# Kernel tuning notes

Measured on AMD Instinct MI355X. Metric: run time of the kernel, lower is better.

The kernel has to match this reference:

```python
import jax, jax.numpy as jnp
import numpy as np
from jax import lax

B, N, T, F_IN = 16, 500, 256, 8
H, K, OUT = 64, 3, 1
EPS = 1e-5


def setup_inputs() -> dict:
    key = jax.random.key(0)
    ks = jax.random.split(key, 20)
    def xavier(k, shape):
        fan_in, fan_out = shape[-2], shape[-1]
        lim = np.sqrt(6.0 / (fan_in + fan_out))
        return jax.random.uniform(k, shape, jnp.float32, -lim, lim)
    inp = {
        'x': jax.random.normal(ks[0], (B, N, T, F_IN), jnp.float32),
        'adj': jax.random.uniform(ks[1], (N, N), jnp.float32),
        # temporal conv layer 1: in=F_IN, layer 2: in=H; kernel (1,K), OIHW
        'conv_w1': jax.random.normal(ks[2], (H, F_IN, 1, K), jnp.float32) * 0.1,
        'conv_b1': jnp.zeros((H,), jnp.float32),
        'conv_w2': jax.random.normal(ks[3], (H, H, 1, K), jnp.float32) * 0.05,
        'conv_b2': jnp.zeros((H,), jnp.float32),
        # graph conv weights (in,out) + bias
        'gcn_w1': xavier(ks[4], (H, H)),
        'gcn_b1': jnp.zeros((H,), jnp.float32),
        'gcn_w2': xavier(ks[5], (H, H)),
        'gcn_b2': jnp.zeros((H,), jnp.float32),
        # batchnorm (eval mode: running stats)
        'bn_g1': jnp.ones((H,), jnp.float32),
        'bn_be1': jnp.zeros((H,), jnp.float32),
        'bn_m1': jax.random.normal(ks[6], (H,), jnp.float32) * 0.1,
        'bn_v1': jnp.ones((H,), jnp.float32),
        'bn_g2': jnp.ones((H,), jnp.float32),
        'bn_be2': jnp.zeros((H,), jnp.float32),
        'bn_m2': jax.random.normal(ks[7], (H,), jnp.float32) * 0.1,
        'bn_v2': jnp.ones((H,), jnp.float32),
        # output MLP H -> H//2 -> OUT
        'out_w1': xavier(ks[8], (H, H // 2)),
        'out_bb1': jnp.zeros((H // 2,), jnp.float32),
        'out_w2': xavier(ks[9], (H // 2, OUT)),
        'out_bb2': jnp.zeros((OUT,), jnp.float32),
    }
    return inp


def _layer(x, adj, cw, cb, gw, gb, bg, bb, bm, bv):
    # x: (B, C_in, N, T)
    x = lax.conv_general_dilated(
        x, cw, window_strides=(1, 1), padding=[(0, 0), (K // 2, K // 2)],
        dimension_numbers=('NCHW', 'OIHW', 'NCHW'))
    x = jax.nn.relu(x + cb[None, :, None, None])           # (B,H,N,T)
    # batched graph conv over all timesteps at once
    s = jnp.einsum('bcnt,ch->bhnt', x, gw)                 # support = x @ W
    x = jnp.einsum('mn,bhnt->bhmt', adj, s) + gb[None, :, None, None]
    x = jax.nn.relu(x)
    # batchnorm2d eval over channel dim
    x = (x - bm[None, :, None, None]) * (bg / jnp.sqrt(bv + EPS))[None, :, None, None] + bb[None, :, None, None]
    return x  # dropout is identity in eval


def reference(x, adj, conv_w1, conv_b1, conv_w2, conv_b2,
              gcn_w1, gcn_b1, gcn_w2, gcn_b2,
              bn_g1, bn_be1, bn_m1, bn_v1,
              bn_g2, bn_be2, bn_m2, bn_v2,
              out_w1, out_bb1, out_w2, out_bb2):
    h = jnp.transpose(x, (0, 3, 1, 2))                      # (B,F_in,N,T)
    h = _layer(h, adj, conv_w1, conv_b1, gcn_w1, gcn_b1, bn_g1, bn_be1, bn_m1, bn_v1)
    h = _layer(h, adj, conv_w2, conv_b2, gcn_w2, gcn_b2, bn_g2, bn_be2, bn_m2, bn_v2)
    h = h.mean(axis=-1)                                     # (B,H,N)
    h = jnp.transpose(h, (0, 2, 1))                         # (B,N,H)
    h = jax.nn.relu(h @ out_w1 + out_bb1)
    return h @ out_w2 + out_bb2                             # (B,N,OUT)
```

## Files before the change

kernel.cpp:

```cpp
#include <hip/hip_runtime.h>
#include <hip/hip_bf16.h>


#define BB 16
#define NN 500
#define TT 256
#define FIN 8
#define HH 64

using bf16 = __hip_bfloat16;
typedef __attribute__((ext_vector_type(8))) short short8;
typedef __attribute__((ext_vector_type(4))) short short4v;
typedef __attribute__((ext_vector_type(4))) float f32x4;

static __device__ __forceinline__ short bf16bits(float v) {
    __hip_bfloat16 h = __float2bfloat16(v);
    return *reinterpret_cast<short*>(&h);
}

__global__ __launch_bounds__(256) void k_prep_adj(
    const float* __restrict__ adj, bf16* __restrict__ adjb)
{
    int i = blockIdx.x * 256 + threadIdx.x;
    if (i < 512 * 512) {
        int r = i >> 9, c = i & 511;
        float v = (r < NN && c < NN) ? adj[r * NN + c] : 0.f;
        adjb[i] = __float2bfloat16(v);
    }
}

__global__ __launch_bounds__(256) void k_prep_weights(
    const float* __restrict__ cw1, const float* __restrict__ gw1,
    const float* __restrict__ w2,  const float* __restrict__ gw2,
    bf16* __restrict__ wA1, bf16* __restrict__ gA1,
    bf16* __restrict__ wA2, bf16* __restrict__ gA2)
{
    int i = blockIdx.x * 256 + threadIdx.x;
    if (i < 2048) {
        int h = i >> 5, kp = i & 31, kk = kp >> 3, f = kp & 7;
        wA1[i] = __float2bfloat16(kk < 3 ? cw1[(h * 8 + f) * 3 + kk] : 0.f);
    } else if (i < 6144) {
        int j = i - 2048, h = j >> 6, c = j & 63;
        gA1[j] = __float2bfloat16(gw1[c * 64 + h]);
    } else if (i < 18432) {
        int j = i - 6144, kk = j / 4096, r = j & 4095, co = r >> 6, ci = r & 63;
        wA2[j] = __float2bfloat16(w2[(co * 64 + ci) * 3 + kk]);
    } else if (i < 22528) {
        int j = i - 18432, h = j >> 6, c = j & 63;
        gA2[j] = __float2bfloat16(gw2[c * 64 + h]);
    }
}

__global__ __launch_bounds__(256) void k_conv_mfma1(
    const float* __restrict__ x, const bf16* __restrict__ wA1,
    const bf16* __restrict__ gA1, const float* __restrict__ cb,
    bf16* __restrict__ s_out)
{
    __shared__ __align__(16) short xs[256 * 64];

    const int tid = threadIdx.x;
    const int n = blockIdx.x, lb = blockIdx.y;
    const int lane = tid & 63, w = tid >> 6;
    const int lr = lane & 15, kg = lane >> 4;
    const int t0w = w * 64;

    {
        const float4* gx = (const float4*)(x + (size_t)(lb * NN + n) * (TT * FIN) + tid * 8);
        float4 a = gx[0], b = gx[1];
        short8 v;
        v[0] = bf16bits(a.x); v[1] = bf16bits(a.y); v[2] = bf16bits(a.z); v[3] = bf16bits(a.w);
        v[4] = bf16bits(b.x); v[5] = bf16bits(b.y); v[6] = bf16bits(b.z); v[7] = bf16bits(b.w);
        const int t = tid;
        *(short8*)((char*)xs + t * 128 + (16 ^ ((t & 7) << 4))) = v;
        if (t < 255)
            *(short8*)((char*)xs + (t + 1) * 128 + (0 ^ (((t + 1) & 7) << 4))) = v;
        if (t > 0)
            *(short8*)((char*)xs + (t - 1) * 128 + (32 ^ (((t - 1) & 7) << 4))) = v;
        short8 z = {0, 0, 0, 0, 0, 0, 0, 0};
        *(short8*)((char*)xs + t * 128 + (48 ^ ((t & 7) << 4))) = z;
        if (t == 0)   *(short8*)((char*)xs + 0 * 128 + (0 ^ 0)) = z;
        if (t == 255) *(short8*)((char*)xs + 255 * 128 + (32 ^ ((255 & 7) << 4))) = z;
    }
    __syncthreads();

    f32x4 acc[4][4];
    #pragma unroll
    for (int mi = 0; mi < 4; mi++)
        #pragma unroll
        for (int ti = 0; ti < 4; ti++)
            acc[mi][ti] = (f32x4){0.f, 0.f, 0.f, 0.f};

    const short* wAp = (const short*)wA1;
    {
        short8 af[4], bfr[4];
        #pragma unroll
        for (int mi = 0; mi < 4; mi++)
            af[mi] = *(const short8*)(wAp + (mi * 16 + lr) * 32 + kg * 8);
        #pragma unroll
        for (int ti = 0; ti < 4; ti++) {
            const int row = t0w + ti * 16 + lr;
            bfr[ti] = *(const short8*)((const char*)xs + row * 128 + ((kg * 16) ^ ((row & 7) << 4)));
        }
        #pragma unroll
        for (int ti = 0; ti < 4; ti++)
            #pragma unroll
            for (int mi = 0; mi < 4; mi++)
                acc[mi][ti] = __builtin_amdgcn_mfma_f32_16x16x32_bf16(af[mi], bfr[ti], acc[mi][ti], 0, 0, 0);
    }
    __syncthreads();

    {
        float cbl[16];
        #pragma unroll
        for (int mi = 0; mi < 4; mi++)
            #pragma unroll
            for (int r = 0; r < 4; r++) cbl[mi * 4 + r] = cb[mi * 16 + kg * 4 + r];
        #pragma unroll
        for (int mi = 0; mi < 4; mi++) {
            #pragma unroll
            for (int ti = 0; ti < 4; ti++) {
                const int t = t0w + ti * 16 + lr;
                short4v yv;
                #pragma unroll
                for (int r = 0; r < 4; r++)
                    yv[r] = bf16bits(fmaxf(acc[mi][ti][r] + cbl[mi * 4 + r], 0.f));
                *(short4v*)((char*)xs + t * 128 + ((mi * 32 + kg * 8) ^ ((t & 7) << 4))) = yv;
            }
        }
    }
    __syncthreads();

    f32x4 acc2[4][4];
    #pragma unroll
    for (int mi = 0; mi < 4; mi++)
        #pragma unroll
        for (int ti = 0; ti < 4; ti++)
            acc2[mi][ti] = (f32x4){0.f, 0.f, 0.f, 0.f};

    const short* gAp = (const short*)gA1;
    #pragma unroll
    for (int ks = 0; ks < 2; ks++) {
        short8 af[4], bfr[4];
        #pragma unroll
        for (int mi = 0; mi < 4; mi++)
            af[mi] = *(const short8*)(gAp + (mi * 16 + lr) * 64 + ks * 32 + kg * 8);
        #pragma unroll
        for (int ti = 0; ti < 4; ti++) {
            const int t = t0w + ti * 16 + lr;
            bfr[ti] = *(const short8*)((const char*)xs + t * 128 + ((ks * 64 + kg * 16) ^ ((t & 7) << 4)));
        }
        #pragma unroll
        for (int ti = 0; ti < 4; ti++)
            #pragma unroll
            for (int mi = 0; mi < 4; mi++)
                acc2[mi][ti] = __builtin_amdgcn_mfma_f32_16x16x32_bf16(af[mi], bfr[ti], acc2[mi][ti], 0, 0, 0);
    }

    #pragma unroll
    for (int mi = 0; mi < 4; mi++) {
        #pragma unroll
        for (int r = 0; r < 4; r++) {
            const int h = mi * 16 + kg * 4 + r;
            bf16* orow = s_out + ((size_t)(lb * 64 + h) * NN + n) * TT + t0w + lr;
            #pragma unroll
            for (int ti = 0; ti < 4; ti++)
                orow[ti * 16] = __float2bfloat16(acc2[mi][ti][r]);
        }
    }
}

#define SWZ_T(t) (((((t) & 7) ^ (((t) >> 5) << 1)) & 7) << 4)

template<bool MEAN>
__global__ __launch_bounds__(512) void k_adj_mfma(
    const bf16* __restrict__ s_in, const bf16* __restrict__ adjb,
    const float* __restrict__ gb, const float* __restrict__ bn_g,
    const float* __restrict__ bn_b, const float* __restrict__ bn_m,
    const float* __restrict__ bn_v, bf16* __restrict__ h_out,
    float* __restrict__ pf, int nbh)
{
    __shared__ __align__(16) short AsS[256 * 72];
    __shared__ __align__(16) short BtS[128 * 64];

    const int tid = threadIdx.x;
    const int id = blockIdx.x;
    const int xcd = id & 7;
    const int jj = id >> 3;
    const int mt = jj & 1;
    const int g = ((jj >> 1) << 3) + xcd;
    const int bh = g >> 1;
    const int m0 = mt * 256;
    const int t0 = (g & 1) * 128;
    const int h = bh & 63;

    const int lane = tid & 63;
    const int lr = lane & 15;
    const int kg = lane >> 4;
    const int w = tid >> 6;
    const int wr = w >> 1, wc = w & 1;

    f32x4 acc[4][4];
    #pragma unroll
    for (int mi = 0; mi < 4; mi++)
        #pragma unroll
        for (int ti = 0; ti < 4; ti++)
            acc[mi][ti] = (f32x4){0.f, 0.f, 0.f, 0.f};

    const int ar = tid >> 1, ah = (tid & 1) * 32;
    const int sk = tid >> 3, tseg = (tid & 7) * 16;
    const bf16* sslice = s_in + (size_t)bh * (NN * TT) + t0;

    for (int rnd = 0; rnd < 8; rnd++) {
        const int k0 = rnd * 64;
        {
            const float4* src = (const float4*)(adjb + (size_t)(m0 + ar) * 512 + k0 + ah);
            float4* dst = (float4*)(AsS + ar * 72 + ah);
            dst[0] = src[0]; dst[1] = src[1]; dst[2] = src[2]; dst[3] = src[3];
        }
        {
            const int kglob = k0 + sk;
            short8 v0, v1;
            if (kglob < NN) {
                const short8* gg = (const short8*)(sslice + (size_t)kglob * TT + tseg);
                v0 = gg[0]; v1 = gg[1];
            } else {
                v0 = (short8){0,0,0,0,0,0,0,0}; v1 = v0;
            }
            const int kslot = (sk >> 3) << 4;
            const int kfine = (sk & 7) * 2;
            #pragma unroll
            for (int u = 0; u < 2; u++) {
                short8 v = (u == 0) ? v0 : v1;
                #pragma unroll
                for (int j = 0; j < 8; j++) {
                    const int t = tseg + u * 8 + j;
                    *(short*)((char*)BtS + t * 128 + (kslot ^ SWZ_T(t)) + kfine) = v[j];
                }
            }
        }
        __syncthreads();

        #pragma unroll
        for (int ks = 0; ks < 2; ks++) {
            short8 af[4], bfr[4];
            #pragma unroll
            for (int mi = 0; mi < 4; mi++)
                af[mi] = *(const short8*)(AsS + (wr * 64 + mi * 16 + lr) * 72 + ks * 32 + kg * 8);
            #pragma unroll
            for (int ti = 0; ti < 4; ti++) {
                const int t = wc * 64 + ti * 16 + lr;
                bfr[ti] = *(const short8*)((const char*)BtS + t * 128 + ((((ks * 4 + kg) << 4)) ^ SWZ_T(t)));
            }
            #pragma unroll
            for (int ti = 0; ti < 4; ti++)
                #pragma unroll
                for (int mi = 0; mi < 4; mi++)
                    acc[mi][ti] = __builtin_amdgcn_mfma_f32_16x16x32_bf16(af[mi], bfr[ti], acc[mi][ti], 0, 0, 0);
        }
        __syncthreads();
    }

    const float bias  = gb[h];
    const float scale = bn_g[h] / sqrtf(bn_v[h] + 1e-5f);
    const float shift = bn_b[h] - bn_m[h] * scale;

    if constexpr (!MEAN) {
        #pragma unroll
        for (int mi = 0; mi < 4; mi++) {
            const int mbase = m0 + wr * 64 + mi * 16 + kg * 4;
            #pragma unroll
            for (int r = 0; r < 4; r++) {
                const int m = mbase + r;
                if (m < NN) {
                    bf16* orow = h_out + ((size_t)bh * NN + m) * TT + t0 + wc * 64 + lr;
                    #pragma unroll
                    for (int ti = 0; ti < 4; ti++) {
                        float v = fmaxf(acc[mi][ti][r] + bias, 0.f);
                        orow[ti * 16] = __float2bfloat16(v * scale + shift);
                    }
                }
            }
        }
    } else {
        float sums[4][4];
        #pragma unroll
        for (int mi = 0; mi < 4; mi++)
            #pragma unroll
            for (int r = 0; r < 4; r++) {
                float s = 0.f;
                #pragma unroll
                for (int ti = 0; ti < 4; ti++)
                    s += fmaxf(acc[mi][ti][r] + bias, 0.f) * scale + shift;
                sums[mi][r] = s;
            }
        #pragma unroll
        for (int off = 1; off < 16; off <<= 1)
            #pragma unroll
            for (int mi = 0; mi < 4; mi++)
                #pragma unroll
                for (int r = 0; r < 4; r++)
                    sums[mi][r] += __shfl_xor(sums[mi][r], off, 64);
        if (lr == 0) {
            const size_t stride = (size_t)nbh * NN;
            float* pfb = pf + ((size_t)((g & 1) * 2 + wc)) * stride + (size_t)bh * NN;
            #pragma unroll
            for (int mi = 0; mi < 4; mi++) {
                const int m = m0 + wr * 64 + mi * 16 + kg * 4;
                if (m < NN) {
                    float4 v = make_float4(sums[mi][0], sums[mi][1], sums[mi][2], sums[mi][3]);
                    *(float4*)(pfb + m) = v;
                }
            }
        }
    }
}

__global__ __launch_bounds__(256) void k_conv_mfma2(
    const bf16* __restrict__ hin, const bf16* __restrict__ wA,
    const bf16* __restrict__ gA, const float* __restrict__ cb,
    bf16* __restrict__ s_out)
{
    __shared__ __align__(16) short xs[258 * 64];

    const int tid = threadIdx.x;
    const int n = blockIdx.x, lb = blockIdx.y;
    const int lane = tid & 63, w = tid >> 6;
    const int lr = lane & 15, kg = lane >> 4;
    const int t0w = w * 64;

    const bf16* base = hin + ((size_t)lb * 64 * NN + n) * TT;

    {
        const int cin = tid >> 2, tq = (tid & 3) * 64;
        const short* gsrc = (const short*)(base + (size_t)cin * (NN * TT) + tq);
        #pragma unroll
        for (int i = 0; i < 8; i++) {
            short8 v = *(const short8*)(gsrc + i * 8);
            #pragma unroll
            for (int j = 0; j < 8; j++) {
                const int row = tq + i * 8 + j + 1;
                const int addr = row * 128 + ((cin * 2) ^ ((row & 7) << 4));
                *(short*)((char*)xs + addr) = v[j];
            }
        }
        if (tid < 64) {
            *(short*)((char*)xs + (tid * 2)) = 0;
            *(short*)((char*)xs + 257 * 128 + ((tid * 2) ^ 16)) = 0;
        }
    }
    __syncthreads();

    f32x4 acc[4][4];
    #pragma unroll
    for (int mi = 0; mi < 4; mi++)
        #pragma unroll
        for (int ti = 0; ti < 4; ti++)
            acc[mi][ti] = (f32x4){0.f, 0.f, 0.f, 0.f};

    const short* wAp = (const short*)wA;
    #pragma unroll
    for (int kk = 0; kk < 3; kk++) {
        #pragma unroll
        for (int ks = 0; ks < 2; ks++) {
            short8 af[4], bfr[4];
            #pragma unroll
            for (int mi = 0; mi < 4; mi++)
                af[mi] = *(const short8*)(wAp + ((kk * 64 + mi * 16 + lr) * 64 + ks * 32 + kg * 8));
            #pragma unroll
            for (int ti = 0; ti < 4; ti++) {
                const int row = t0w + ti * 16 + lr + kk;
                const int addr = row * 128 + ((ks * 64 + kg * 16) ^ ((row & 7) << 4));
                bfr[ti] = *(const short8*)((const char*)xs + addr);
            }
            #pragma unroll
            for (int ti = 0; ti < 4; ti++)
                #pragma unroll
                for (int mi = 0; mi < 4; mi++)
                    acc[mi][ti] = __builtin_amdgcn_mfma_f32_16x16x32_bf16(af[mi], bfr[ti], acc[mi][ti], 0, 0, 0);
        }
    }
    __syncthreads();

    {
        float cbl[16];
        #pragma unroll
        for (int mi = 0; mi < 4; mi++)
            #pragma unroll
            for (int r = 0; r < 4; r++) cbl[mi * 4 + r] = cb[mi * 16 + kg * 4 + r];
        #pragma unroll
        for (int mi = 0; mi < 4; mi++) {
            #pragma unroll
            for (int ti = 0; ti < 4; ti++) {
                const int t = t0w + ti * 16 + lr;
                short4v yv;
                #pragma unroll
                for (int r = 0; r < 4; r++)
                    yv[r] = bf16bits(fmaxf(acc[mi][ti][r] + cbl[mi * 4 + r], 0.f));
                const int addr = t * 128 + ((mi * 32 + kg * 8) ^ ((t & 7) << 4));
                *(short4v*)((char*)xs + addr) = yv;
            }
        }
    }
    __syncthreads();

    f32x4 acc2[4][4];
    #pragma unroll
    for (int mi = 0; mi < 4; mi++)
        #pragma unroll
        for (int ti = 0; ti < 4; ti++)
            acc2[mi][ti] = (f32x4){0.f, 0.f, 0.f, 0.f};

    const short* gAp = (const short*)gA;
    #pragma unroll
    for (int ks = 0; ks < 2; ks++) {
        short8 af[4], bfr[4];
        #pragma unroll
        for (int mi = 0; mi < 4; mi++)
            af[mi] = *(const short8*)(gAp + ((mi * 16 + lr) * 64 + ks * 32 + kg * 8));
        #pragma unroll
        for (int ti = 0; ti < 4; ti++) {
            const int t = t0w + ti * 16 + lr;
            const int addr = t * 128 + ((ks * 64 + kg * 16) ^ ((t & 7) << 4));
            bfr[ti] = *(const short8*)((const char*)xs + addr);
        }
        #pragma unroll
        for (int ti = 0; ti < 4; ti++)
            #pragma unroll
            for (int mi = 0; mi < 4; mi++)
                acc2[mi][ti] = __builtin_amdgcn_mfma_f32_16x16x32_bf16(af[mi], bfr[ti], acc2[mi][ti], 0, 0, 0);
    }

    #pragma unroll
    for (int mi = 0; mi < 4; mi++) {
        #pragma unroll
        for (int r = 0; r < 4; r++) {
            const int h = mi * 16 + kg * 4 + r;
            bf16* orow = s_out + ((size_t)(lb * 64 + h) * NN + n) * TT + t0w + lr;
            #pragma unroll
            for (int ti = 0; ti < 4; ti++)
                orow[ti * 16] = __float2bfloat16(acc2[mi][ti][r]);
        }
    }
}

__global__ __launch_bounds__(64) void k_mlp(
    const float* __restrict__ pf, int nbh,
    const float* __restrict__ w1, const float* __restrict__ b1,
    const float* __restrict__ w2, const float* __restrict__ b2,
    float* __restrict__ out)
{
    __shared__ float mm[64];
    __shared__ float hid[32];
    const int n = blockIdx.x, lb = blockIdx.y, tid = threadIdx.x;

    const size_t stride = (size_t)nbh * NN;
    const size_t idx = (size_t)(lb * 64 + tid) * NN + n;
    float s = pf[idx] + pf[stride + idx] + pf[2 * stride + idx] + pf[3 * stride + idx];
    mm[tid] = s * (1.f / 256.f);
    __syncthreads();
    if (tid < 32) {
        float a = b1[tid];
        #pragma unroll
        for (int c = 0; c < 64; c++) a += mm[c] * w1[c * 32 + tid];
        hid[tid] = fmaxf(a, 0.f);
    }
    __syncthreads();
    if (tid == 0) {
        float a = b2[0];
        #pragma unroll
        for (int j = 0; j < 32; j++) a += hid[j] * w2[j];
        out[lb * NN + n] = a;
    }
}

extern "C" void kernel_launch(void* const* d_in, const int* in_sizes, int n_in,
                              void* d_out, int out_size, void* d_ws, size_t ws_size,
                              hipStream_t stream) {
    const float* x       = (const float*)d_in[0];
    const float* adj     = (const float*)d_in[1];
    const float* conv_w1 = (const float*)d_in[2];
    const float* conv_b1 = (const float*)d_in[3];
    const float* conv_w2 = (const float*)d_in[4];
    const float* conv_b2 = (const float*)d_in[5];
    const float* gcn_w1  = (const float*)d_in[6];
    const float* gcn_b1  = (const float*)d_in[7];
    const float* gcn_w2  = (const float*)d_in[8];
    const float* gcn_b2  = (const float*)d_in[9];
    const float* bn_g1   = (const float*)d_in[10];
    const float* bn_be1  = (const float*)d_in[11];
    const float* bn_m1   = (const float*)d_in[12];
    const float* bn_v1   = (const float*)d_in[13];
    const float* bn_g2   = (const float*)d_in[14];
    const float* bn_be2  = (const float*)d_in[15];
    const float* bn_m2   = (const float*)d_in[16];
    const float* bn_v2   = (const float*)d_in[17];
    const float* out_w1  = (const float*)d_in[18];
    const float* out_b1  = (const float*)d_in[19];
    const float* out_w2  = (const float*)d_in[20];
    const float* out_b2  = (const float*)d_in[21];
    float* out = (float*)d_out;

    const size_t per_b = (size_t)HH * NN * TT;
    const size_t reserve = 1 << 20;
    const size_t bytes_per_b_both = per_b * 2 * 2;
    int chunk = (int)((ws_size > reserve ? ws_size - reserve : 0) / bytes_per_b_both);
    if (chunk > BB) chunk = BB;
    if (chunk < 1) chunk = 1;

    char* ws = (char*)d_ws;
    bf16* adjb = (bf16*)ws;
    bf16* wA2  = (bf16*)(ws + 0x80000);
    bf16* gA2  = (bf16*)(ws + 0x80000 + 24576);
    bf16* wA1  = (bf16*)(ws + 0x80000 + 32768);
    bf16* gA1  = (bf16*)(ws + 0x80000 + 36864);
    bf16* bufA = (bf16*)(ws + reserve);
    bf16* bufB = bufA + (size_t)chunk * per_b;

    k_prep_adj<<<1024, 256, 0, stream>>>(adj, adjb);
    k_prep_weights<<<88, 256, 0, stream>>>(conv_w1, gcn_w1, conv_w2, gcn_w2,
                                           wA1, gA1, wA2, gA2);

    for (int b0 = 0; b0 < BB; b0 += chunk) {
        const int nb = (BB - b0) < chunk ? (BB - b0) : chunk;
        const int nbh = nb * 64;
        float* pf = (float*)bufB;

        k_conv_mfma1<<<dim3(NN, nb), 256, 0, stream>>>(
            x + (size_t)b0 * NN * TT * FIN, wA1, gA1, conv_b1, bufA);

        k_adj_mfma<false><<<dim3(4 * nbh), 512, 0, stream>>>(
            bufA, adjb, gcn_b1, bn_g1, bn_be1, bn_m1, bn_v1, bufB, nullptr, nbh);

        k_conv_mfma2<<<dim3(NN, nb), 256, 0, stream>>>(
            bufB, wA2, gA2, conv_b2, bufA);

        k_adj_mfma<true><<<dim3(4 * nbh), 512, 0, stream>>>(
            bufA, adjb, gcn_b2, bn_g2, bn_be2, bn_m2, bn_v2, nullptr, pf, nbh);

        k_mlp<<<dim3(NN, nb), 64, 0, stream>>>(
            pf, nbh, out_w1, out_b1, out_w2, out_b2, out + (size_t)b0 * NN);
    }
}
```

Measured before the change: 662.2 us.

## Split second conv kernel into two time halves per block with halo loads

The second temporal-conv kernel now launches two blocks per node/batch, each covering 128 timesteps instead of 256. This halves shared memory per block and accumulator registers per thread, aiming for higher occupancy and more blocks to hide latency. Halo timesteps at the split boundary are loaded from global memory, and the LDS swizzle is changed to also mix in higher row bits. The cost is redundant halo loads and more blocks to schedule.

```diff
diff --git a/kernel.cpp b/kernel.cpp
--- a/kernel.cpp
+++ b/kernel.cpp
@@ -315,46 +315,53 @@
     }
 }
 
+#define SWZ2(row) (((((row) & 7) ^ ((((row) >> 5) & 3) << 1)) & 7) << 4)
+
 __global__ __launch_bounds__(256) void k_conv_mfma2(
     const bf16* __restrict__ hin, const bf16* __restrict__ wA,
     const bf16* __restrict__ gA, const float* __restrict__ cb,
     bf16* __restrict__ s_out)
 {
-    __shared__ __align__(16) short xs[258 * 64];
+    __shared__ __align__(16) short xs[130 * 64];
 
     const int tid = threadIdx.x;
-    const int n = blockIdx.x, lb = blockIdx.y;
+    const int th = blockIdx.x;
+    const int n = blockIdx.y, lb = blockIdx.z;
     const int lane = tid & 63, w = tid >> 6;
     const int lr = lane & 15, kg = lane >> 4;
-    const int t0w = w * 64;
+    const int wt0 = w * 32;
+    const int t0 = th * 128;
 
     const bf16* base = hin + ((size_t)lb * 64 * NN + n) * TT;
 
     {
-        const int cin = tid >> 2, tq = (tid & 3) * 64;
-        const short* gsrc = (const short*)(base + (size_t)cin * (NN * TT) + tq);
-        #pragma unroll
-        for (int i = 0; i < 8; i++) {
+        const int cin = tid >> 2, tq = (tid & 3) * 32;
+        const short* gsrc = (const short*)(base + (size_t)cin * (NN * TT) + t0 + tq);
+        #pragma unroll
+        for (int i = 0; i < 4; i++) {
             short8 v = *(const short8*)(gsrc + i * 8);
             #pragma unroll
             for (int j = 0; j < 8; j++) {
                 const int row = tq + i * 8 + j + 1;
-                const int addr = row * 128 + ((cin * 2) ^ ((row & 7) << 4));
-                *(short*)((char*)xs + addr) = v[j];
+                *(short*)((char*)xs + row * 128 + ((cin * 2) ^ SWZ2(row))) = v[j];
             }
         }
         if (tid < 64) {
-            *(short*)((char*)xs + (tid * 2)) = 0;
-            *(short*)((char*)xs + 257 * 128 + ((tid * 2) ^ 16)) = 0;
-        }
-    }
-    __syncthreads();
-
-    f32x4 acc[4][4];
+            const int cin2 = tid;
+            short v0 = 0, v1 = 0;
+            if (th == 1) v0 = ((const short*)(base + (size_t)cin2 * (NN * TT)))[127];
+            if (th == 0) v1 = ((const short*)(base + (size_t)cin2 * (NN * TT)))[128];
+            *(short*)((char*)xs + 0 * 128 + ((cin2 * 2) ^ SWZ2(0))) = v0;
+            *(short*)((char*)xs + 129 * 128 + ((cin2 * 2) ^ SWZ2(129))) = v1;
+        }
+    }
+    __syncthreads();
+
+    f32x4 acc[4][2];
     #pragma unroll
     for (int mi = 0; mi < 4; mi++)
         #pragma unroll
-        for (int ti = 0; ti < 4; ti++)
+        for (int ti = 0; ti < 2; ti++)
             acc[mi][ti] = (f32x4){0.f, 0.f, 0.f, 0.f};
 
     const short* wAp = (const short*)wA;
@@ -362,18 +369,17 @@
     for (int kk = 0; kk < 3; kk++) {
         #pragma unroll
         for (int ks = 0; ks < 2; ks++) {
-            short8 af[4], bfr[4];
+            short8 af[4], bfr[2];
             #pragma unroll
             for (int mi = 0; mi < 4; mi++)
                 af[mi] = *(const short8*)(wAp + ((kk * 64 + mi * 16 + lr) * 64 + ks * 32 + kg * 8));
             #pragma unroll
-            for (int ti = 0; ti < 4; ti++) {
-                const int row = t0w + ti * 16 + lr + kk;
-                const int addr = row * 128 + ((ks * 64 + kg * 16) ^ ((row & 7) << 4));
-                bfr[ti] = *(const short8*)((const char*)xs + addr);
-            }
-            #pragma unroll
-            for (int ti = 0; ti < 4; ti++)
+            for (int ti = 0; ti < 2; ti++) {
+                const int row = wt0 + ti * 16 + lr + kk;
+                bfr[ti] = *(const short8*)((const char*)xs + row * 128 + ((ks * 64 + kg * 16) ^ SWZ2(row)));
+            }
+            #pragma unroll
+            for (int ti = 0; ti < 2; ti++)
                 #pragma unroll
                 for (int mi = 0; mi < 4; mi++)
                     acc[mi][ti] = __builtin_amdgcn_mfma_f32_16x16x32_bf16(af[mi], bfr[ti], acc[mi][ti], 0, 0, 0);
@@ -390,41 +396,39 @@
         #pragma unroll
         for (int mi = 0; mi < 4; mi++) {
             #pragma unroll
-            for (int ti = 0; ti < 4; ti++) {
-                const int t = t0w + ti * 16 + lr;
+            for (int ti = 0; ti < 2; ti++) {
+                const int t = wt0 + ti * 16 + lr;
                 short4v yv;
                 #pragma unroll
                 for (int r = 0; r < 4; r++)
                     yv[r] = bf16bits(fmaxf(acc[mi][ti][r] + cbl[mi * 4 + r], 0.f));
-                const int addr = t * 128 + ((mi * 32 + kg * 8) ^ ((t & 7) << 4));
-                *(short4v*)((char*)xs + addr) = yv;
-            }
-        }
-    }
-    __syncthreads();
-
-    f32x4 acc2[4][4];
+                *(short4v*)((char*)xs + t * 128 + ((mi * 32 + kg * 8) ^ SWZ2(t))) = yv;
+            }
+        }
+    }
+    __syncthreads();
+
+    f32x4 acc2[4][2];
     #pragma unroll
     for (int mi = 0; mi < 4; mi++)
         #pragma unroll
-        for (int ti = 0; ti < 4; ti++)
+        for (int ti = 0; ti < 2; ti++)
             acc2[mi][ti] = (f32x4){0.f, 0.f, 0.f, 0.f};
 
     const short* gAp = (const short*)gA;
     #pragma unroll
     for (int ks = 0; ks < 2; ks++) {
-        short8 af[4], bfr[4];
+        short8 af[4], bfr[2];
         #pragma unroll
         for (int mi = 0; mi < 4; mi++)
             af[mi] = *(const short8*)(gAp + ((mi * 16 + lr) * 64 + ks * 32 + kg * 8));
         #pragma unroll
-        for (int ti = 0; ti < 4; ti++) {
-            const int t = t0w + ti * 16 + lr;
-            const int addr = t * 128 + ((ks * 64 + kg * 16) ^ ((t & 7) << 4));
-            bfr[ti] = *(const short8*)((const char*)xs + addr);
-        }
-        #pragma unroll
-        for (int ti = 0; ti < 4; ti++)
+        for (int ti = 0; ti < 2; ti++) {
+            const int t = wt0 + ti * 16 + lr;
+            bfr[ti] = *(const short8*)((const char*)xs + t * 128 + ((ks * 64 + kg * 16) ^ SWZ2(t)));
+        }
+        #pragma unroll
+        for (int ti = 0; ti < 2; ti++)
             #pragma unroll
             for (int mi = 0; mi < 4; mi++)
                 acc2[mi][ti] = __builtin_amdgcn_mfma_f32_16x16x32_bf16(af[mi], bfr[ti], acc2[mi][ti], 0, 0, 0);
@@ -435,9 +439,9 @@
         #pragma unroll
         for (int r = 0; r < 4; r++) {
             const int h = mi * 16 + kg * 4 + r;
-            bf16* orow = s_out + ((size_t)(lb * 64 + h) * NN + n) * TT + t0w + lr;
-            #pragma unroll
-            for (int ti = 0; ti < 4; ti++)
+            bf16* orow = s_out + ((size_t)(lb * 64 + h) * NN + n) * TT + t0 + wt0 + lr;
+            #pragma unroll
+            for (int ti = 0; ti < 2; ti++)
                 orow[ti * 16] = __float2bfloat16(acc2[mi][ti][r]);
         }
     }
@@ -531,7 +535,7 @@
         k_adj_mfma<false><<<dim3(4 * nbh), 512, 0, stream>>>(
             bufA, adjb, gcn_b1, bn_g1, bn_be1, bn_m1, bn_v1, bufB, nullptr, nbh);
 
-        k_conv_mfma2<<<dim3(NN, nb), 256, 0, stream>>>(
+        k_conv_mfma2<<<dim3(2, NN, nb), 256, 0, stream>>>(
             bufB, wA2, gA2, conv_b2, bufA);
 
         k_adj_mfma<true><<<dim3(4 * nbh), 512, 0, stream>>>(
```

After: 750.0 us. 13.3% more time.
